# Kernel tuning notes

Hardware: AMD Instinct MI355X
Metric: run time of the kernel (lower is better)

The kernel has to match this reference:

```python
import jax, jax.numpy as jnp
import numpy as np

B, T, N, F_IN = 4, 16, 1000, 8
E = 8000
HID = 64
HEADS = 4
L = 5


def setup_inputs() -> dict:
    key = jax.random.key(0)
    ks = jax.random.split(key, 16)
    s = 0.1
    return {
        "x_seq": jax.random.normal(ks[0], (B, T, N, F_IN), dtype=jnp.float32),
        "edge_index": jax.random.randint(ks[1], (2, E), 0, N, dtype=jnp.int32),
        "edge_weight": jax.random.uniform(ks[2], (E,), dtype=jnp.float32),
        # input projection
        "W_in": jax.random.normal(ks[3], (F_IN, HID)) * s,
        "b_in": jnp.zeros((HID,), jnp.float32),
        # 5 stacked GATConv layers (heads=4, concat=False -> per-head dim = HID, mean over heads)
        "Wg": jax.random.normal(ks[4], (L, HID, HEADS * HID)) * s,
        "a_src": jax.random.normal(ks[5], (L, HEADS, HID)) * s,
        "a_dst": jax.random.normal(ks[6], (L, HEADS, HID)) * s,
        "bg": jnp.zeros((L, HID), jnp.float32),
        # GRU (input = N*HID flattened node features, torch gate order r,z,n)
        "W_ih": jax.random.normal(ks[7], (3 * HID, N * HID)) * 0.02,
        "W_hh": jax.random.normal(ks[8], (3 * HID, HID)) * s,
        "b_ih": jnp.zeros((3 * HID,), jnp.float32),
        "b_hh": jnp.zeros((3 * HID,), jnp.float32),
        # head: Linear(hidden_dim, num_nodes*pred_window) so out.view(B, N) works
        "W_fc": jax.random.normal(ks[9], (HID, N)) * s,
        "b_fc": jnp.zeros((N,), jnp.float32),
    }


def reference(x_seq, edge_index, edge_weight, W_in, b_in, Wg, a_src, a_dst, bg,
              W_ih, W_hh, b_ih, b_hh, W_fc, b_fc):
    Bb, Tt, Nn, Fin = x_seq.shape
    hid = W_in.shape[1]
    heads = a_src.shape[1]
    # PyG GATConv adds self-loops by default
    self_loops = jnp.arange(Nn, dtype=edge_index.dtype)
    src = jnp.concatenate([edge_index[0], self_loops])
    dst = jnp.concatenate([edge_index[1], self_loops])

    # input_fc over all (batch*seq*node) rows
    x = (x_seq.reshape(-1, Fin) @ W_in + b_in).reshape(Bb * Tt, Nn, hid)

    def gat_one(x_g, W, asrc, adst, b):
        h = (x_g @ W).reshape(Nn, heads, hid)            # [N,H,C]
        ls = (h * asrc).sum(-1)                          # [N,H] src attention terms
        ld = (h * adst).sum(-1)                          # [N,H] dst attention terms
        e = jax.nn.leaky_relu(ls[src] + ld[dst], 0.2)    # [E',H]
        m = jax.ops.segment_max(e, dst, num_segments=Nn)
        ex = jnp.exp(e - m[dst])
        den = jax.ops.segment_sum(ex, dst, num_segments=Nn)
        alpha = ex / (den[dst] + 1e-16)                  # softmax over incoming edges
        msg = alpha[:, :, None] * h[src]                 # [E',H,C]
        agg = jax.ops.segment_sum(msg, dst, num_segments=Nn)
        return agg.mean(axis=1) + b                      # concat=False -> mean heads

    for l in range(Wg.shape[0]):
        x = jax.nn.elu(jax.vmap(
            lambda xg, W=Wg[l], a1=a_src[l], a2=a_dst[l], b=bg[l]: gat_one(xg, W, a1, a2, b)
        )(x))

    # GRU over time, input = flattened node features per timestep
    seq = x.reshape(Bb, Tt, Nn * hid).transpose(1, 0, 2)  # [T,B,N*HID]

    def step(h, x_t):
        gi = x_t @ W_ih.T + b_ih
        gh = h @ W_hh.T + b_hh
        ir, iz, inn = jnp.split(gi, 3, axis=-1)
        hr, hz, hn = jnp.split(gh, 3, axis=-1)
        r = jax.nn.sigmoid(ir + hr)
        z = jax.nn.sigmoid(iz + hz)
        n = jnp.tanh(inn + r * hn)
        return (1.0 - z) * n + z * h, None

    h0 = jnp.zeros((Bb, hid), x_seq.dtype)
    hT, _ = jax.lax.scan(step, h0, seq)                  # last GRU output == final h
    return hT @ W_fc + b_fc                              # [B, N]
```

## Files before the change

### kernel.cpp

```cpp
#include <hip/hip_runtime.h>
#include <math.h>

#define NB 4
#define TT 16
#define NNODE 1000
#define FIN 8
#define EE 8000
#define EP 9000
#define EPAD 16384
#define HID 64
#define HEADS 4
#define NL 5
#define GG (NB*TT)
#define ROWS (GG*NNODE)
#define HCOL (HEADS*HID)
#define KGI (NNODE*HID)
#define GOUT 192
#define GIK 128
#define KSPLIT (KGI/GIK)
#define GOSZ (GG*GOUT)
#define WPSZ (8*4*64*8)

typedef unsigned short u16;
typedef __attribute__((ext_vector_type(8))) short short8;
typedef __attribute__((ext_vector_type(4))) float f32x4;

__device__ inline u16 f2bf(float f) {
    unsigned int u = __float_as_uint(f);
    unsigned int r = u + 0x7FFFu + ((u >> 16) & 1u);
    return (u16)(r >> 16);
}
__device__ inline float bf2f(u16 h) {
    return __uint_as_float(((unsigned int)h) << 16);
}
__device__ inline ushort4 bfhi4(float4 a) {
    ushort4 r; r.x = f2bf(a.x); r.y = f2bf(a.y); r.z = f2bf(a.z); r.w = f2bf(a.w); return r;
}
__device__ inline ushort4 bflo4(float4 a, ushort4 h) {
    ushort4 r;
    r.x = f2bf(a.x - bf2f(h.x)); r.y = f2bf(a.y - bf2f(h.y));
    r.z = f2bf(a.z - bf2f(h.z)); r.w = f2bf(a.w - bf2f(h.w));
    return r;
}

__global__ void k_build_edges(const int* __restrict__ eidx, int* __restrict__ src_e,
                              int* __restrict__ dst_e, int* __restrict__ deg, int* __restrict__ fill) {
    int i = blockIdx.x * blockDim.x + threadIdx.x;
    if (i < EP) {
        int s, d;
        if (i < EE) { s = eidx[i]; d = eidx[EE + i]; }
        else { s = i - EE; d = i - EE; }
        src_e[i] = s; dst_e[i] = d;
    }
    if (i < NNODE) { deg[i] = 0; fill[i] = 0; }
}

__global__ void k_csr_count(const int* __restrict__ dst_e, int* __restrict__ deg) {
    int i = blockIdx.x * blockDim.x + threadIdx.x;
    if (i < EP) atomicAdd(&deg[dst_e[i]], 1);
}

__global__ __launch_bounds__(256) void k_csr_scan(const int* __restrict__ deg, int* __restrict__ rowptr_p) {
    __shared__ int s[1024];
    int tid = threadIdx.x;
    for (int i = tid; i < 1024; i += 256) s[i] = (i < NNODE) ? ((deg[i] + 7) & ~7) : 0;
    __syncthreads();
    for (int off = 1; off < 1024; off <<= 1) {
        int t[4];
        #pragma unroll
        for (int q = 0; q < 4; q++) { int i = tid + 256 * q; t[q] = (i >= off) ? s[i - off] : 0; }
        __syncthreads();
        #pragma unroll
        for (int q = 0; q < 4; q++) { int i = tid + 256 * q; s[i] += t[q]; }
        __syncthreads();
    }
    for (int i = tid; i < NNODE; i += 256) rowptr_p[i + 1] = s[i];
    if (tid == 0) rowptr_p[0] = 0;
}

__global__ void k_csr_fill(const int* __restrict__ src_e, const int* __restrict__ dst_e,
                           const int* __restrict__ rowptr_p, const int* __restrict__ deg,
                           int* __restrict__ fill, int* __restrict__ csr_src) {
    int i = blockIdx.x * blockDim.x + threadIdx.x;
    if (i < EP) {
        int d = dst_e[i];
        int pos = atomicAdd(&fill[d], 1);
        csr_src[rowptr_p[d] + pos] = src_e[i];
    }
    if (i < NNODE) {
        int rs = rowptr_p[i], re = rowptr_p[i + 1];
        for (int j = rs + deg[i]; j < re; j++) csr_src[j] = i;
    }
}

__global__ void k_wa(const float* __restrict__ Wg, const float* __restrict__ a_src,
                     const float* __restrict__ a_dst, float* __restrict__ wa, float* __restrict__ wd) {
    int t = blockIdx.x * 256 + threadIdx.x;
    if (t >= 2 * NL * HID * HEADS) return;
    int kind = t >= NL * HID * HEADS;
    int u = t - kind * NL * HID * HEADS;
    int l = u >> 8;
    int rem = u & 255;
    int j = rem >> 2, hd = rem & 3;
    const float* a = (kind ? a_dst : a_src) + (size_t)l * HCOL + hd * HID;
    const float* Wl = Wg + (size_t)l * HID * HCOL + (size_t)j * HCOL + hd * HID;
    float acc = 0.f;
    #pragma unroll 8
    for (int c = 0; c < HID; c++) acc += Wl[c] * a[c];
    float* out = kind ? wd : wa;
    out[(size_t)l * HCOL + j * 4 + hd] = acc;
}

__global__ void k_wpack(const float* __restrict__ Wg, u16* __restrict__ wph, u16* __restrict__ wpl) {
    int t = blockIdx.x * 256 + threadIdx.x;
    if (t >= NL * WPSZ) return;
    int j    = t & 7;
    int lane = (t >> 3) & 63;
    int ct   = (t >> 9) & 3;
    int ks   = (t >> 11) & 7;
    int l    = t >> 14;
    int k = ks * 32 + (lane >> 4) * 8 + j;
    int c = ct * 16 + (lane & 15);
    float v = Wg[(size_t)l * HID * HCOL + (size_t)(k & 63) * HCOL + (k >> 6) * 64 + c];
    u16 h = f2bf(v);
    wph[t] = h;
    wpl[t] = f2bf(v - bf2f(h));
}

__global__ void k_input_fc(const float* __restrict__ xseq, const float4* __restrict__ Win4,
                           const float4* __restrict__ b_in4, const float4* __restrict__ wa04,
                           const float4* __restrict__ wd04, float4* __restrict__ x0,
                           float4* __restrict__ ls4, float4* __restrict__ ld4) {
    int idx = blockIdx.x * 256 + threadIdx.x;
    int r = idx >> 4, c4 = idx & 15;
    float4 acc = b_in4[c4];
    #pragma unroll
    for (int k = 0; k < FIN; k++) {
        float xv = xseq[r * FIN + k];
        float4 w = Win4[k * 16 + c4];
        acc.x += xv * w.x; acc.y += xv * w.y; acc.z += xv * w.z; acc.w += xv * w.w;
    }
    x0[idx] = acc;
    float xr[4] = {acc.x, acc.y, acc.z, acc.w};
    float4 pls = make_float4(0.f, 0.f, 0.f, 0.f);
    float4 pld = make_float4(0.f, 0.f, 0.f, 0.f);
    #pragma unroll
    for (int jj = 0; jj < 4; jj++) {
        float4 wa_j = wa04[c4 * 4 + jj];
        float4 wd_j = wd04[c4 * 4 + jj];
        pls.x += xr[jj] * wa_j.x; pls.y += xr[jj] * wa_j.y;
        pls.z += xr[jj] * wa_j.z; pls.w += xr[jj] * wa_j.w;
        pld.x += xr[jj] * wd_j.x; pld.y += xr[jj] * wd_j.y;
        pld.z += xr[jj] * wd_j.z; pld.w += xr[jj] * wd_j.w;
    }
    #pragma unroll
    for (int o = 1; o < 16; o <<= 1) {
        pls.x += __shfl_xor(pls.x, o, 64); pls.y += __shfl_xor(pls.y, o, 64);
        pls.z += __shfl_xor(pls.z, o, 64); pls.w += __shfl_xor(pls.w, o, 64);
        pld.x += __shfl_xor(pld.x, o, 64); pld.y += __shfl_xor(pld.y, o, 64);
        pld.z += __shfl_xor(pld.z, o, 64); pld.w += __shfl_xor(pld.w, o, 64);
    }
    if (c4 == 0) {
        ls4[r] = pls;
        ld4[r] = pld;
    }
}

__global__ __launch_bounds__(256) void k_aggx(const float4* __restrict__ x4, const float4* __restrict__ ls4,
                                              const float4* __restrict__ ld4, const int* __restrict__ rowptr_p,
                                              const int* __restrict__ csr_src, const int* __restrict__ deg,
                                              u16* __restrict__ yh, u16* __restrict__ yl) {
    __shared__ float s_e[4][4][264];
    __shared__ int   s_src[4][4][64];
    __shared__ float s_den[4][4][4];
    int b = blockIdx.x;
    int xcd = b & 7, s = b >> 3;
    int tid = threadIdx.x;
    int wid = tid >> 6, lane = tid & 63;
    int w = s * 4 + wid;
    int g = xcd + 8 * (w / 250);
    int n0 = (w % 250) * 4;
    int nsub = lane >> 4;
    int j0 = lane & 15;
    int n_s = n0 + nsub;
    int rs = rowptr_p[n_s];
    int dgp = rowptr_p[n_s + 1] - rs;
    int dg = deg[n_s];
    int dg16 = (dgp + 15) & ~15;
    if (dg16 > 64) dg16 = 64;
    if (dgp > 64) dgp = 64;
    if (dg > 64) dg = 64;
    float4 ldv = ld4[(size_t)g * NNODE + n_s];
    const float4* lsg = ls4 + (size_t)g * NNODE;

    float4 mx = make_float4(-1e30f, -1e30f, -1e30f, -1e30f);
    for (int base = 0; base < dg16; base += 16) {
        int j = base + j0;
        int sv = n_s;
        if (j < dgp) sv = csr_src[rs + j];
        s_src[wid][nsub][j] = sv;
        float4 lo = make_float4(-1e30f, -1e30f, -1e30f, -1e30f);
        if (j < dg) {
            float4 t = lsg[sv];
            t.x += ldv.x; t.y += ldv.y; t.z += ldv.z; t.w += ldv.w;
            t.x = fmaxf(t.x, 0.2f * t.x); t.y = fmaxf(t.y, 0.2f * t.y);
            t.z = fmaxf(t.z, 0.2f * t.z); t.w = fmaxf(t.w, 0.2f * t.w);
            lo = t;
            mx.x = fmaxf(mx.x, lo.x); mx.y = fmaxf(mx.y, lo.y);
            mx.z = fmaxf(mx.z, lo.z); mx.w = fmaxf(mx.w, lo.w);
        }
        *reinterpret_cast<float4*>(&s_e[wid][nsub][j * 4]) = lo;
    }
    #pragma unroll
    for (int o = 1; o < 16; o <<= 1) {
        mx.x = fmaxf(mx.x, __shfl_xor(mx.x, o, 64));
        mx.y = fmaxf(mx.y, __shfl_xor(mx.y, o, 64));
        mx.z = fmaxf(mx.z, __shfl_xor(mx.z, o, 64));
        mx.w = fmaxf(mx.w, __shfl_xor(mx.w, o, 64));
    }
    float4 den = make_float4(0.f, 0.f, 0.f, 0.f);
    for (int base = 0; base < dg16; base += 16) {
        int j = base + j0;
        float4 e = make_float4(0.f, 0.f, 0.f, 0.f);
        if (j < dg) {
            float4 lo = *reinterpret_cast<const float4*>(&s_e[wid][nsub][j * 4]);
            e.x = __expf(lo.x - mx.x);
            e.y = __expf(lo.y - mx.y);
            e.z = __expf(lo.z - mx.z);
            e.w = __expf(lo.w - mx.w);
        }
        den.x += e.x; den.y += e.y; den.z += e.z; den.w += e.w;
        *reinterpret_cast<float4*>(&s_e[wid][nsub][j * 4]) = e;
    }
    #pragma unroll
    for (int o = 1; o < 16; o <<= 1) {
        den.x += __shfl_xor(den.x, o, 64);
        den.y += __shfl_xor(den.y, o, 64);
        den.z += __shfl_xor(den.z, o, 64);
        den.w += __shfl_xor(den.w, o, 64);
    }
    if (j0 == 0) {
        *reinterpret_cast<float4*>(&s_den[wid][nsub][0]) = den;
    }

    int c4 = lane & 15;
    const float4* xg = x4 + (size_t)g * NNODE * 16 + c4;
    float4 a0 = make_float4(0.f, 0.f, 0.f, 0.f);
    float4 a1 = a0, a2 = a0, a3 = a0;
    const float* ep = &s_e[wid][nsub][0];
    const int* sp = &s_src[wid][nsub][0];
    int dg4 = (dg + 3) & ~3;
    int q = 0;
    for (; q + 8 <= dg4; q += 8) {
        int sj[8]; float4 ev[8], xv[8];
        #pragma unroll
        for (int u = 0; u < 8; u++) sj[u] = sp[q + u];
        #pragma unroll
        for (int u = 0; u < 8; u++) xv[u] = xg[(size_t)sj[u] * 16];
        #pragma unroll
        for (int u = 0; u < 8; u++) ev[u] = *reinterpret_cast<const float4*>(&ep[(q + u) * 4]);
        #pragma unroll
        for (int u = 0; u < 8; u++) {
            a0.x += ev[u].x * xv[u].x; a0.y += ev[u].x * xv[u].y;
            a0.z += ev[u].x * xv[u].z; a0.w += ev[u].x * xv[u].w;
            a1.x += ev[u].y * xv[u].x; a1.y += ev[u].y * xv[u].y;
            a1.z += ev[u].y * xv[u].z; a1.w += ev[u].y * xv[u].w;
            a2.x += ev[u].z * xv[u].x; a2.y += ev[u].z * xv[u].y;
            a2.z += ev[u].z * xv[u].z; a2.w += ev[u].z * xv[u].w;
            a3.x += ev[u].w * xv[u].x; a3.y += ev[u].w * xv[u].y;
            a3.z += ev[u].w * xv[u].z; a3.w += ev[u].w * xv[u].w;
        }
    }
    if (q < dg4) {
        int sj[4]; float4 ev[4], xv[4];
        #pragma unroll
        for (int u = 0; u < 4; u++) sj[u] = sp[q + u];
        #pragma unroll
        for (int u = 0; u < 4; u++) xv[u] = xg[(size_t)sj[u] * 16];
        #pragma unroll
        for (int u = 0; u < 4; u++) ev[u] = *reinterpret_cast<const float4*>(&ep[(q + u) * 4]);
        #pragma unroll
        for (int u = 0; u < 4; u++) {
            a0.x += ev[u].x * xv[u].x; a0.y += ev[u].x * xv[u].y;
            a0.z += ev[u].x * xv[u].z; a0.w += ev[u].x * xv[u].w;
            a1.x += ev[u].y * xv[u].x; a1.y += ev[u].y * xv[u].y;
            a1.z += ev[u].y * xv[u].z; a1.w += ev[u].y * xv[u].w;
            a2.x += ev[u].z * xv[u].x; a2.y += ev[u].z * xv[u].y;
            a2.z += ev[u].z * xv[u].z; a2.w += ev[u].z * xv[u].w;
            a3.x += ev[u].w * xv[u].x; a3.y += ev[u].w * xv[u].y;
            a3.z += ev[u].w * xv[u].z; a3.w += ev[u].w * xv[u].w;
        }
    }
    float4 dv = *reinterpret_cast<const float4*>(&s_den[wid][nsub][0]);
    float i0 = 1.f / (dv.x + 1e-16f), i1 = 1.f / (dv.y + 1e-16f);
    float i2 = 1.f / (dv.z + 1e-16f), i3 = 1.f / (dv.w + 1e-16f);
    a0.x *= i0; a0.y *= i0; a0.z *= i0; a0.w *= i0;
    a1.x *= i1; a1.y *= i1; a1.z *= i1; a1.w *= i1;
    a2.x *= i2; a2.y *= i2; a2.z *= i2; a2.w *= i2;
    a3.x *= i3; a3.y *= i3; a3.z *= i3; a3.w *= i3;
    size_t wb = ((size_t)g * NNODE + n_s) * 64 + c4;
    ushort4* YH = reinterpret_cast<ushort4*>(yh);
    ushort4* YL = reinterpret_cast<ushort4*>(yl);
    ushort4 h0 = bfhi4(a0), h1 = bfhi4(a1), h2 = bfhi4(a2), h3 = bfhi4(a3);
    YH[wb +  0] = h0; YL[wb +  0] = bflo4(a0, h0);
    YH[wb + 16] = h1; YL[wb + 16] = bflo4(a1, h1);
    YH[wb + 32] = h2; YL[wb + 32] = bflo4(a2, h2);
    YH[wb + 48] = h3; YL[wb + 48] = bflo4(a3, h3);
}

__global__ __launch_bounds__(256) void k_ygemm_mfma(const u16* __restrict__ yh, const u16* __restrict__ yl,
                                                    const u16* __restrict__ wph, const u16* __restrict__ wpl,
                                                    const float* __restrict__ bg, float* __restrict__ xout,
                                                    const float4* __restrict__ wa4, const float4* __restrict__ wd4,
                                                    float4* __restrict__ ls4, float4* __restrict__ ld4) {
    int tid = threadIdx.x;
    int wv = tid >> 6, lane = tid & 63;
    int r0w = blockIdx.x * 64 + wv * 16;
    int arow = lane & 15, kg = lane >> 4;

    f32x4 acc0 = {0.f, 0.f, 0.f, 0.f};
    f32x4 acc1 = {0.f, 0.f, 0.f, 0.f};
    f32x4 acc2 = {0.f, 0.f, 0.f, 0.f};
    f32x4 acc3 = {0.f, 0.f, 0.f, 0.f};

    const short8* ah8 = reinterpret_cast<const short8*>(yh + (size_t)(r0w + arow) * 256 + kg * 8);
    const short8* al8 = reinterpret_cast<const short8*>(yl + (size_t)(r0w + arow) * 256 + kg * 8);
    const short8* bh8 = reinterpret_cast<const short8*>(wph) + lane;
    const short8* bl8 = reinterpret_cast<const short8*>(wpl) + lane;

    #pragma unroll
    for (int ks = 0; ks < 8; ks++) {
        short8 ah = ah8[ks * 4];
        short8 al = al8[ks * 4];
        #pragma unroll
        for (int ct = 0; ct < 4; ct++) {
            short8 bh = bh8[(size_t)(ks * 4 + ct) * 64];
            short8 bl = bl8[(size_t)(ks * 4 + ct) * 64];
            f32x4* ac = (ct == 0) ? &acc0 : (ct == 1) ? &acc1 : (ct == 2) ? &acc2 : &acc3;
            *ac = __builtin_amdgcn_mfma_f32_16x16x32_bf16(ah, bh, *ac, 0, 0, 0);
            *ac = __builtin_amdgcn_mfma_f32_16x16x32_bf16(ah, bl, *ac, 0, 0, 0);
            *ac = __builtin_amdgcn_mfma_f32_16x16x32_bf16(al, bh, *ac, 0, 0, 0);
        }
    }

    float ev[4][4];
    #pragma unroll
    for (int ct = 0; ct < 4; ct++) {
        int c = ct * 16 + arow;
        float bc = bg[c];
        f32x4 a = (ct == 0) ? acc0 : (ct == 1) ? acc1 : (ct == 2) ? acc2 : acc3;
        #pragma unroll
        for (int r = 0; r < 4; r++) {
            float v = a[r] * 0.25f + bc;
            float e = v > 0.f ? v : expm1f(v);
            ev[ct][r] = e;
            xout[(size_t)(r0w + kg * 4 + r) * HID + c] = e;
        }
    }
    if (wa4) {
        #pragma unroll
        for (int r = 0; r < 4; r++) {
            float4 pls = make_float4(0.f, 0.f, 0.f, 0.f);
            float4 pld = make_float4(0.f, 0.f, 0.f, 0.f);
            #pragma unroll
            for (int ct = 0; ct < 4; ct++) {
                int c = ct * 16 + arow;
                float e = ev[ct][r];
                float4 wa_c = wa4[c];
                float4 wd_c = wd4[c];
                pls.x += e * wa_c.x; pls.y += e * wa_c.y;
                pls.z += e * wa_c.z; pls.w += e * wa_c.w;
                pld.x += e * wd_c.x; pld.y += e * wd_c.y;
                pld.z += e * wd_c.z; pld.w += e * wd_c.w;
            }
            #pragma unroll
            for (int o = 1; o < 16; o <<= 1) {
                pls.x += __shfl_xor(pls.x, o, 64); pls.y += __shfl_xor(pls.y, o, 64);
                pls.z += __shfl_xor(pls.z, o, 64); pls.w += __shfl_xor(pls.w, o, 64);
                pld.x += __shfl_xor(pld.x, o, 64); pld.y += __shfl_xor(pld.y, o, 64);
                pld.z += __shfl_xor(pld.z, o, 64); pld.w += __shfl_xor(pld.w, o, 64);
            }
            if (arow == 0) {
                int row = r0w + kg * 4 + r;
                ls4[row] = pls;
                ld4[row] = pld;
            }
        }
    }
}

__global__ __launch_bounds__(256) void k_gi_gemm(const float* __restrict__ x, const float* __restrict__ W_ih,
                                                 float* __restrict__ gip) {
    __shared__ float xs[32 * 68];
    __shared__ float ws[32 * 196];
    int k0 = blockIdx.x * GIK;
    int tid = threadIdx.x;
    int lane = tid & 63;
    int wv = tid >> 6;
    int tx = tid & 15, ty = tid >> 4;
    float4 accs[4][3];
    #pragma unroll
    for (int i = 0; i < 4; i++)
        #pragma unroll
        for (int j = 0; j < 3; j++) accs[i][j] = make_float4(0.f, 0.f, 0.f, 0.f);

    for (int kt = 0; kt < GIK / 32; kt++) {
        int kb = k0 + kt * 32;
        #pragma unroll
        for (int it = 0; it < 2; it++) {
            int kq = wv + 4 * it;
            float4 v = *reinterpret_cast<const float4*>(&x[(size_t)lane * KGI + kb + kq * 4]);
            int k = kq * 4;
            xs[(k + 0) * 68 + lane] = v.x;
            xs[(k + 1) * 68 + lane] = v.y;
            xs[(k + 2) * 68 + lane] = v.z;
            xs[(k + 3) * 68 + lane] = v.w;
        }
        #pragma unroll
        for (int cg = 0; cg < 3; cg++) {
            #pragma unroll
            for (int it = 0; it < 2; it++) {
                int kq = wv + 4 * it;
                int c = cg * 64 + lane;
                float4 v = *reinterpret_cast<const float4*>(&W_ih[(size_t)c * KGI + kb + kq * 4]);
                int k = kq * 4;
                ws[(k + 0) * 196 + c] = v.x;
                ws[(k + 1) * 196 + c] = v.y;
                ws[(k + 2) * 196 + c] = v.z;
                ws[(k + 3) * 196 + c] = v.w;
            }
        }
        __syncthreads();
        for (int kk = 0; kk < 32; kk++) {
            float4 xv = *reinterpret_cast<const float4*>(&xs[kk * 68 + ty * 4]);
            float4 w0 = *reinterpret_cast<const float4*>(&ws[kk * 196 + tx * 4]);
            float4 w1 = *reinterpret_cast<const float4*>(&ws[kk * 196 + 64 + tx * 4]);
            float4 w2 = *reinterpret_cast<const float4*>(&ws[kk * 196 + 128 + tx * 4]);
            #pragma unroll
            for (int i = 0; i < 4; i++) {
                float xi = (i == 0) ? xv.x : (i == 1) ? xv.y : (i == 2) ? xv.z : xv.w;
                accs[i][0].x += xi * w0.x; accs[i][0].y += xi * w0.y; accs[i][0].z += xi * w0.z; accs[i][0].w += xi * w0.w;
                accs[i][1].x += xi * w1.x; accs[i][1].y += xi * w1.y; accs[i][1].z += xi * w1.z; accs[i][1].w += xi * w1.w;
                accs[i][2].x += xi * w2.x; accs[i][2].y += xi * w2.y; accs[i][2].z += xi * w2.z; accs[i][2].w += xi * w2.w;
            }
        }
        __syncthreads();
    }
    float* out = gip + (size_t)blockIdx.x * GOSZ;
    #pragma unroll
    for (int i = 0; i < 4; i++)
        #pragma unroll
        for (int j = 0; j < 3; j++)
            *reinterpret_cast<float4*>(&out[(ty * 4 + i) * GOUT + j * 64 + tx * 4]) = accs[i][j];
}

__global__ void k_gi_reduce1(const float* __restrict__ gip, float* __restrict__ gip2) {
    int idx = blockIdx.x * 256 + threadIdx.x;
    const float* p = gip + (size_t)blockIdx.y * 50 * GOSZ + idx;
    float a = 0.f;
    #pragma unroll 5
    for (int s = 0; s < 50; s++) a += p[(size_t)s * GOSZ];
    gip2[blockIdx.y * GOSZ + idx] = a;
}

__global__ void k_gi_reduce2(const float* __restrict__ gip2, const float* __restrict__ b_ih,
                             float* __restrict__ gi) {
    int idx = blockIdx.x * 256 + threadIdx.x;
    float a = b_ih[idx % GOUT];
    #pragma unroll
    for (int y = 0; y < 10; y++) a += gip2[(size_t)y * GOSZ + idx];
    gi[idx] = a;
}

__global__ __launch_bounds__(192) void k_gru(const float* __restrict__ gi, const float* __restrict__ W_hh,
                                             const float* __restrict__ b_hh, float* __restrict__ hT) {
    __shared__ float hs[64];
    __shared__ float gh[192];
    int j = threadIdx.x;
    int b = blockIdx.x;
    float wrow[64];
    #pragma unroll
    for (int q = 0; q < 16; q++) {
        float4 v = *reinterpret_cast<const float4*>(&W_hh[(size_t)j * 64 + q * 4]);
        wrow[q * 4 + 0] = v.x; wrow[q * 4 + 1] = v.y;
        wrow[q * 4 + 2] = v.z; wrow[q * 4 + 3] = v.w;
    }
    float bj = b_hh[j];
    if (j < 64) hs[j] = 0.f;
    __syncthreads();
    for (int t = 0; t < TT; t++) {
        float a0 = 0.f, a1 = 0.f, a2 = 0.f, a3 = 0.f;
        #pragma unroll
        for (int q = 0; q < 16; q++) {
            float4 h4 = *reinterpret_cast<const float4*>(&hs[q * 4]);
            a0 += h4.x * wrow[q * 4 + 0];
            a1 += h4.y * wrow[q * 4 + 1];
            a2 += h4.z * wrow[q * 4 + 2];
            a3 += h4.w * wrow[q * 4 + 3];
        }
        gh[j] = bj + ((a0 + a1) + (a2 + a3));
        __syncthreads();
        if (j < 64) {
            int row = (b * TT + t) * GOUT;
            float ir = gi[row + j], iz = gi[row + 64 + j], in_ = gi[row + 128 + j];
            float r = 1.f / (1.f + expf(-(ir + gh[j])));
            float z = 1.f / (1.f + expf(-(iz + gh[64 + j])));
            float nv = tanhf(in_ + r * gh[128 + j]);
            hs[j] = (1.f - z) * nv + z * hs[j];
        }
        __syncthreads();
    }
    if (j < 64) hT[b * 64 + j] = hs[j];
}

__global__ void k_final(const float* __restrict__ hT, const float* __restrict__ W_fc,
                        const float* __restrict__ b_fc, float* __restrict__ out) {
    int idx = blockIdx.x * 256 + threadIdx.x;
    if (idx >= NB * NNODE) return;
    int b = idx / NNODE, n = idx % NNODE;
    float acc = b_fc[n];
    #pragma unroll
    for (int c = 0; c < HID; c++) acc += hT[b * HID + c] * W_fc[c * NNODE + n];
    out[idx] = acc;
}

extern "C" void kernel_launch(void* const* d_in, const int* in_sizes, int n_in,
                              void* d_out, int out_size, void* d_ws, size_t ws_size,
                              hipStream_t stream) {
    const float* x_seq  = (const float*)d_in[0];
    const int*   eidx   = (const int*)  d_in[1];
    const float* W_in   = (const float*)d_in[3];
    const float* b_in   = (const float*)d_in[4];
    const float* Wg     = (const float*)d_in[5];
    const float* a_src  = (const float*)d_in[6];
    const float* a_dst  = (const float*)d_in[7];
    const float* bg     = (const float*)d_in[8];
    const float* W_ih   = (const float*)d_in[9];
    const float* W_hh   = (const float*)d_in[10];
    const float* b_ih   = (const float*)d_in[11];
    const float* b_hh   = (const float*)d_in[12];
    const float* W_fc   = (const float*)d_in[13];
    const float* b_fc   = (const float*)d_in[14];
    float* out = (float*)d_out;

    float* wsf = (float*)d_ws;
    size_t off = 0;
    float* x0     = wsf + off; off += (size_t)ROWS * HID;
    float* ybuf   = wsf + off; off += (size_t)ROWS * HCOL;
    float* lsb    = wsf + off; off += (size_t)ROWS * HEADS;
    float* ldb    = wsf + off; off += (size_t)ROWS * HEADS;
    float* wab    = wsf + off; off += NL * HCOL;
    float* wdb    = wsf + off; off += NL * HCOL;
    float* gib    = wsf + off; off += GOSZ;
    float* hTb    = wsf + off; off += 256;
    u16* wphb     = (u16*)(wsf + off); off += NL * WPSZ / 2;
    u16* wplb     = (u16*)(wsf + off); off += NL * WPSZ / 2;
    int* ib = (int*)(wsf + off);
    int* src_e    = ib;          ib += EP;
    int* dst_e    = ib;          ib += EP;
    int* rowptr_p = ib;          ib += NNODE + 1;
    int* csr_src  = ib;          ib += EPAD;
    int* deg      = ib;          ib += NNODE;
    int* fill     = ib;          ib += NNODE;

    u16* yh = (u16*)ybuf;
    u16* yl = yh + (size_t)ROWS * HCOL;

    float* gip  = ybuf;
    float* gip2 = ybuf + (size_t)KSPLIT * GOSZ;

    k_build_edges<<<(EP + 255) / 256, 256, 0, stream>>>(eidx, src_e, dst_e, deg, fill);
    k_csr_count<<<(EP + 255) / 256, 256, 0, stream>>>(dst_e, deg);
    k_csr_scan<<<1, 256, 0, stream>>>(deg, rowptr_p);
    k_csr_fill<<<(EP + 255) / 256, 256, 0, stream>>>(src_e, dst_e, rowptr_p, deg, fill, csr_src);

    k_wa<<<10, 256, 0, stream>>>(Wg, a_src, a_dst, wab, wdb);
    k_wpack<<<(NL * WPSZ + 255) / 256, 256, 0, stream>>>(Wg, wphb, wplb);

    k_input_fc<<<ROWS * 16 / 256, 256, 0, stream>>>(
        x_seq, (const float4*)W_in, (const float4*)b_in,
        (const float4*)wab, (const float4*)wdb, (float4*)x0, (float4*)lsb, (float4*)ldb);

    for (int l = 0; l < NL; l++) {
        k_aggx<<<ROWS / 16, 256, 0, stream>>>(
            (const float4*)x0, (const float4*)lsb, (const float4*)ldb, rowptr_p, csr_src, deg,
            yh, yl);
        const float4* wa_next = (l + 1 < NL) ? (const float4*)(wab + (size_t)(l + 1) * HCOL) : nullptr;
        const float4* wd_next = (l + 1 < NL) ? (const float4*)(wdb + (size_t)(l + 1) * HCOL) : nullptr;
        k_ygemm_mfma<<<ROWS / 64, 256, 0, stream>>>(
            yh, yl, wphb + (size_t)l * WPSZ, wplb + (size_t)l * WPSZ,
            bg + (size_t)l * HID, x0,
            wa_next, wd_next, (float4*)lsb, (float4*)ldb);
    }

    k_gi_gemm<<<KSPLIT, 256, 0, stream>>>(x0, W_ih, gip);
    k_gi_reduce1<<<dim3(GOSZ / 256, 10), 256, 0, stream>>>(gip, gip2);
    k_gi_reduce2<<<GOSZ / 256, 256, 0, stream>>>(gip2, b_ih, gib);
    k_gru<<<4, 192, 0, stream>>>(gib, W_hh, b_hh, hTb);
    k_final<<<(NB * NNODE + 255) / 256, 256, 0, stream>>>(hTb, W_fc, b_fc, out);
}
```

Measured before the change: 432.4 us.

## Fuse GAT aggregation and MFMA projection into one kernel per layer

```diff
diff --git a/kernel.cpp b/kernel.cpp
--- a/kernel.cpp
+++ b/kernel.cpp
@@ -166,206 +166,208 @@
     }
 }
 
-__global__ __launch_bounds__(256) void k_aggx(const float4* __restrict__ x4, const float4* __restrict__ ls4,
-                                              const float4* __restrict__ ld4, const int* __restrict__ rowptr_p,
-                                              const int* __restrict__ csr_src, const int* __restrict__ deg,
-                                              u16* __restrict__ yh, u16* __restrict__ yl) {
+__global__ __launch_bounds__(256) void k_gat_fused(
+        const float4* __restrict__ x4, const float4* __restrict__ ls4, const float4* __restrict__ ld4,
+        const int* __restrict__ rowptr_p, const int* __restrict__ csr_src, const int* __restrict__ deg,
+        const u16* __restrict__ wph, const u16* __restrict__ wpl, const float* __restrict__ bg,
+        float* __restrict__ xout, const float4* __restrict__ wa4, const float4* __restrict__ wd4,
+        float4* __restrict__ lso4, float4* __restrict__ ldo4) {
+    __shared__ u16 yhs[32][264];
+    __shared__ u16 yls[32][264];
     __shared__ float s_e[4][4][264];
-    __shared__ int   s_src[4][4][64];
+    __shared__ unsigned short s_src[4][4][64];
     __shared__ float s_den[4][4][4];
     int b = blockIdx.x;
-    int xcd = b & 7, s = b >> 3;
+    int xcd = b & 7, sb = b >> 3;
+    int g = xcd + 8 * (sb >> 5);
+    int nb = (sb & 31) * 32;
     int tid = threadIdx.x;
     int wid = tid >> 6, lane = tid & 63;
-    int w = s * 4 + wid;
-    int g = xcd + 8 * (w / 250);
-    int n0 = (w % 250) * 4;
     int nsub = lane >> 4;
     int j0 = lane & 15;
-    int n_s = n0 + nsub;
-    int rs = rowptr_p[n_s];
-    int dgp = rowptr_p[n_s + 1] - rs;
-    int dg = deg[n_s];
-    int dg16 = (dgp + 15) & ~15;
-    if (dg16 > 64) dg16 = 64;
-    if (dgp > 64) dgp = 64;
-    if (dg > 64) dg = 64;
-    float4 ldv = ld4[(size_t)g * NNODE + n_s];
+    int c4 = lane & 15;
     const float4* lsg = ls4 + (size_t)g * NNODE;
-
-    float4 mx = make_float4(-1e30f, -1e30f, -1e30f, -1e30f);
-    for (int base = 0; base < dg16; base += 16) {
-        int j = base + j0;
-        int sv = n_s;
-        if (j < dgp) sv = csr_src[rs + j];
-        s_src[wid][nsub][j] = sv;
-        float4 lo = make_float4(-1e30f, -1e30f, -1e30f, -1e30f);
-        if (j < dg) {
-            float4 t = lsg[sv];
-            t.x += ldv.x; t.y += ldv.y; t.z += ldv.z; t.w += ldv.w;
-            t.x = fmaxf(t.x, 0.2f * t.x); t.y = fmaxf(t.y, 0.2f * t.y);
-            t.z = fmaxf(t.z, 0.2f * t.z); t.w = fmaxf(t.w, 0.2f * t.w);
-            lo = t;
-            mx.x = fmaxf(mx.x, lo.x); mx.y = fmaxf(mx.y, lo.y);
-            mx.z = fmaxf(mx.z, lo.z); mx.w = fmaxf(mx.w, lo.w);
-        }
-        *reinterpret_cast<float4*>(&s_e[wid][nsub][j * 4]) = lo;
-    }
-    #pragma unroll
-    for (int o = 1; o < 16; o <<= 1) {
-        mx.x = fmaxf(mx.x, __shfl_xor(mx.x, o, 64));
-        mx.y = fmaxf(mx.y, __shfl_xor(mx.y, o, 64));
-        mx.z = fmaxf(mx.z, __shfl_xor(mx.z, o, 64));
-        mx.w = fmaxf(mx.w, __shfl_xor(mx.w, o, 64));
-    }
-    float4 den = make_float4(0.f, 0.f, 0.f, 0.f);
-    for (int base = 0; base < dg16; base += 16) {
-        int j = base + j0;
-        float4 e = make_float4(0.f, 0.f, 0.f, 0.f);
-        if (j < dg) {
-            float4 lo = *reinterpret_cast<const float4*>(&s_e[wid][nsub][j * 4]);
-            e.x = __expf(lo.x - mx.x);
-            e.y = __expf(lo.y - mx.y);
-            e.z = __expf(lo.z - mx.z);
-            e.w = __expf(lo.w - mx.w);
-        }
-        den.x += e.x; den.y += e.y; den.z += e.z; den.w += e.w;
-        *reinterpret_cast<float4*>(&s_e[wid][nsub][j * 4]) = e;
-    }
-    #pragma unroll
-    for (int o = 1; o < 16; o <<= 1) {
-        den.x += __shfl_xor(den.x, o, 64);
-        den.y += __shfl_xor(den.y, o, 64);
-        den.z += __shfl_xor(den.z, o, 64);
-        den.w += __shfl_xor(den.w, o, 64);
-    }
-    if (j0 == 0) {
-        *reinterpret_cast<float4*>(&s_den[wid][nsub][0]) = den;
-    }
-
-    int c4 = lane & 15;
     const float4* xg = x4 + (size_t)g * NNODE * 16 + c4;
-    float4 a0 = make_float4(0.f, 0.f, 0.f, 0.f);
-    float4 a1 = a0, a2 = a0, a3 = a0;
-    const float* ep = &s_e[wid][nsub][0];
-    const int* sp = &s_src[wid][nsub][0];
-    int dg4 = (dg + 3) & ~3;
-    int q = 0;
-    for (; q + 8 <= dg4; q += 8) {
-        int sj[8]; float4 ev[8], xv[8];
-        #pragma unroll
-        for (int u = 0; u < 8; u++) sj[u] = sp[q + u];
-        #pragma unroll
-        for (int u = 0; u < 8; u++) xv[u] = xg[(size_t)sj[u] * 16];
-        #pragma unroll
-        for (int u = 0; u < 8; u++) ev[u] = *reinterpret_cast<const float4*>(&ep[(q + u) * 4]);
-        #pragma unroll
-        for (int u = 0; u < 8; u++) {
-            a0.x += ev[u].x * xv[u].x; a0.y += ev[u].x * xv[u].y;
-            a0.z += ev[u].x * xv[u].z; a0.w += ev[u].x * xv[u].w;
-            a1.x += ev[u].y * xv[u].x; a1.y += ev[u].y * xv[u].y;
-            a1.z += ev[u].y * xv[u].z; a1.w += ev[u].y * xv[u].w;
-            a2.x += ev[u].z * xv[u].x; a2.y += ev[u].z * xv[u].y;
-            a2.z += ev[u].z * xv[u].z; a2.w += ev[u].z * xv[u].w;
-            a3.x += ev[u].w * xv[u].x; a3.y += ev[u].w * xv[u].y;
-            a3.z += ev[u].w * xv[u].z; a3.w += ev[u].w * xv[u].w;
-        }
-    }
-    if (q < dg4) {
-        int sj[4]; float4 ev[4], xv[4];
-        #pragma unroll
-        for (int u = 0; u < 4; u++) sj[u] = sp[q + u];
-        #pragma unroll
-        for (int u = 0; u < 4; u++) xv[u] = xg[(size_t)sj[u] * 16];
-        #pragma unroll
-        for (int u = 0; u < 4; u++) ev[u] = *reinterpret_cast<const float4*>(&ep[(q + u) * 4]);
-        #pragma unroll
-        for (int u = 0; u < 4; u++) {
-            a0.x += ev[u].x * xv[u].x; a0.y += ev[u].x * xv[u].y;
-            a0.z += ev[u].x * xv[u].z; a0.w += ev[u].x * xv[u].w;
-            a1.x += ev[u].y * xv[u].x; a1.y += ev[u].y * xv[u].y;
-            a1.z += ev[u].y * xv[u].z; a1.w += ev[u].y * xv[u].w;
-            a2.x += ev[u].z * xv[u].x; a2.y += ev[u].z * xv[u].y;
-            a2.z += ev[u].z * xv[u].z; a2.w += ev[u].z * xv[u].w;
-            a3.x += ev[u].w * xv[u].x; a3.y += ev[u].w * xv[u].y;
-            a3.z += ev[u].w * xv[u].z; a3.w += ev[u].w * xv[u].w;
-        }
-    }
-    float4 dv = *reinterpret_cast<const float4*>(&s_den[wid][nsub][0]);
-    float i0 = 1.f / (dv.x + 1e-16f), i1 = 1.f / (dv.y + 1e-16f);
-    float i2 = 1.f / (dv.z + 1e-16f), i3 = 1.f / (dv.w + 1e-16f);
-    a0.x *= i0; a0.y *= i0; a0.z *= i0; a0.w *= i0;
-    a1.x *= i1; a1.y *= i1; a1.z *= i1; a1.w *= i1;
-    a2.x *= i2; a2.y *= i2; a2.z *= i2; a2.w *= i2;
-    a3.x *= i3; a3.y *= i3; a3.z *= i3; a3.w *= i3;
-    size_t wb = ((size_t)g * NNODE + n_s) * 64 + c4;
-    ushort4* YH = reinterpret_cast<ushort4*>(yh);
-    ushort4* YL = reinterpret_cast<ushort4*>(yl);
-    ushort4 h0 = bfhi4(a0), h1 = bfhi4(a1), h2 = bfhi4(a2), h3 = bfhi4(a3);
-    YH[wb +  0] = h0; YL[wb +  0] = bflo4(a0, h0);
-    YH[wb + 16] = h1; YL[wb + 16] = bflo4(a1, h1);
-    YH[wb + 32] = h2; YL[wb + 32] = bflo4(a2, h2);
-    YH[wb + 48] = h3; YL[wb + 48] = bflo4(a3, h3);
-}
-
-__global__ __launch_bounds__(256) void k_ygemm_mfma(const u16* __restrict__ yh, const u16* __restrict__ yl,
-                                                    const u16* __restrict__ wph, const u16* __restrict__ wpl,
-                                                    const float* __restrict__ bg, float* __restrict__ xout,
-                                                    const float4* __restrict__ wa4, const float4* __restrict__ wd4,
-                                                    float4* __restrict__ ls4, float4* __restrict__ ld4) {
-    int tid = threadIdx.x;
-    int wv = tid >> 6, lane = tid & 63;
-    int r0w = blockIdx.x * 64 + wv * 16;
+
+    for (int it2 = 0; it2 < 2; it2++) {
+        __syncthreads();
+        int n_l = wid * 8 + it2 * 4 + nsub;
+        int n_s = nb + n_l;
+        int valid = n_s < NNODE;
+        int n_c = valid ? n_s : (NNODE - 1);
+        int rs = rowptr_p[n_c];
+        int dgp = valid ? (rowptr_p[n_c + 1] - rs) : 0;
+        int dg = valid ? deg[n_c] : 0;
+        int dg16 = (dgp + 15) & ~15;
+        if (dg16 > 64) dg16 = 64;
+        if (dgp > 64) dgp = 64;
+        if (dg > 64) dg = 64;
+        float4 ldv = ld4[(size_t)g * NNODE + n_c];
+
+        float4 mx = make_float4(-1e30f, -1e30f, -1e30f, -1e30f);
+        for (int base = 0; base < dg16; base += 16) {
+            int j = base + j0;
+            int sv = n_c;
+            if (j < dgp) sv = csr_src[rs + j];
+            s_src[wid][nsub][j] = (unsigned short)sv;
+            float4 lo = make_float4(-1e30f, -1e30f, -1e30f, -1e30f);
+            if (j < dg) {
+                float4 t = lsg[sv];
+                t.x += ldv.x; t.y += ldv.y; t.z += ldv.z; t.w += ldv.w;
+                t.x = fmaxf(t.x, 0.2f * t.x); t.y = fmaxf(t.y, 0.2f * t.y);
+                t.z = fmaxf(t.z, 0.2f * t.z); t.w = fmaxf(t.w, 0.2f * t.w);
+                lo = t;
+                mx.x = fmaxf(mx.x, lo.x); mx.y = fmaxf(mx.y, lo.y);
+                mx.z = fmaxf(mx.z, lo.z); mx.w = fmaxf(mx.w, lo.w);
+            }
+            *reinterpret_cast<float4*>(&s_e[wid][nsub][j * 4]) = lo;
+        }
+        #pragma unroll
+        for (int o = 1; o < 16; o <<= 1) {
+            mx.x = fmaxf(mx.x, __shfl_xor(mx.x, o, 64));
+            mx.y = fmaxf(mx.y, __shfl_xor(mx.y, o, 64));
+            mx.z = fmaxf(mx.z, __shfl_xor(mx.z, o, 64));
+            mx.w = fmaxf(mx.w, __shfl_xor(mx.w, o, 64));
+        }
+        float4 den = make_float4(0.f, 0.f, 0.f, 0.f);
+        for (int base = 0; base < dg16; base += 16) {
+            int j = base + j0;
+            float4 e = make_float4(0.f, 0.f, 0.f, 0.f);
+            if (j < dg) {
+                float4 lo = *reinterpret_cast<const float4*>(&s_e[wid][nsub][j * 4]);
+                e.x = __expf(lo.x - mx.x);
+                e.y = __expf(lo.y - mx.y);
+                e.z = __expf(lo.z - mx.z);
+                e.w = __expf(lo.w - mx.w);
+            }
+            den.x += e.x; den.y += e.y; den.z += e.z; den.w += e.w;
+            *reinterpret_cast<float4*>(&s_e[wid][nsub][j * 4]) = e;
+        }
+        #pragma unroll
+        for (int o = 1; o < 16; o <<= 1) {
+            den.x += __shfl_xor(den.x, o, 64);
+            den.y += __shfl_xor(den.y, o, 64);
+            den.z += __shfl_xor(den.z, o, 64);
+            den.w += __shfl_xor(den.w, o, 64);
+        }
+        if (j0 == 0) *reinterpret_cast<float4*>(&s_den[wid][nsub][0]) = den;
+        __syncthreads();
+
+        float4 a0 = make_float4(0.f, 0.f, 0.f, 0.f);
+        float4 a1 = a0, a2 = a0, a3 = a0;
+        const float* ep = &s_e[wid][nsub][0];
+        const unsigned short* sp = &s_src[wid][nsub][0];
+        int dg4 = (dg + 3) & ~3;
+        int q = 0;
+        for (; q + 8 <= dg4; q += 8) {
+            int sj[8]; float4 ev[8], xv[8];
+            #pragma unroll
+            for (int u = 0; u < 8; u++) sj[u] = sp[q + u];
+            #pragma unroll
+            for (int u = 0; u < 8; u++) xv[u] = xg[(size_t)sj[u] * 16];
+            #pragma unroll
+            for (int u = 0; u < 8; u++) ev[u] = *reinterpret_cast<const float4*>(&ep[(q + u) * 4]);
+            #pragma unroll
+            for (int u = 0; u < 8; u++) {
+                a0.x += ev[u].x * xv[u].x; a0.y += ev[u].x * xv[u].y;
+                a0.z += ev[u].x * xv[u].z; a0.w += ev[u].x * xv[u].w;
+                a1.x += ev[u].y * xv[u].x; a1.y += ev[u].y * xv[u].y;
+                a1.z += ev[u].y * xv[u].z; a1.w += ev[u].y * xv[u].w;
+                a2.x += ev[u].z * xv[u].x; a2.y += ev[u].z * xv[u].y;
+                a2.z += ev[u].z * xv[u].z; a2.w += ev[u].z * xv[u].w;
+                a3.x += ev[u].w * xv[u].x; a3.y += ev[u].w * xv[u].y;
+                a3.z += ev[u].w * xv[u].z; a3.w += ev[u].w * xv[u].w;
+            }
+        }
+        if (q < dg4) {
+            int sj[4]; float4 ev[4], xv[4];
+            #pragma unroll
+            for (int u = 0; u < 4; u++) sj[u] = sp[q + u];
+            #pragma unroll
+            for (int u = 0; u < 4; u++) xv[u] = xg[(size_t)sj[u] * 16];
+            #pragma unroll
+            for (int u = 0; u < 4; u++) ev[u] = *reinterpret_cast<const float4*>(&ep[(q + u) * 4]);
+            #pragma unroll
+            for (int u = 0; u < 4; u++) {
+                a0.x += ev[u].x * xv[u].x; a0.y += ev[u].x * xv[u].y;
+                a0.z += ev[u].x * xv[u].z; a0.w += ev[u].x * xv[u].w;
+                a1.x += ev[u].y * xv[u].x; a1.y += ev[u].y * xv[u].y;
+                a1.z += ev[u].y * xv[u].z; a1.w += ev[u].y * xv[u].w;
+                a2.x += ev[u].z * xv[u].x; a2.y += ev[u].z * xv[u].y;
+                a2.z += ev[u].z * xv[u].z; a2.w += ev[u].z * xv[u].w;
+                a3.x += ev[u].w * xv[u].x; a3.y += ev[u].w * xv[u].y;
+                a3.z += ev[u].w * xv[u].z; a3.w += ev[u].w * xv[u].w;
+            }
+        }
+        float4 dv = *reinterpret_cast<const float4*>(&s_den[wid][nsub][0]);
+        float i0 = 1.f / (dv.x + 1e-16f), i1 = 1.f / (dv.y + 1e-16f);
+        float i2 = 1.f / (dv.z + 1e-16f), i3 = 1.f / (dv.w + 1e-16f);
+        a0.x *= i0; a0.y *= i0; a0.z *= i0; a0.w *= i0;
+        a1.x *= i1; a1.y *= i1; a1.z *= i1; a1.w *= i1;
+        a2.x *= i2; a2.y *= i2; a2.z *= i2; a2.w *= i2;
+        a3.x *= i3; a3.y *= i3; a3.z *= i3; a3.w *= i3;
+        ushort4 h0 = bfhi4(a0), h1 = bfhi4(a1), h2 = bfhi4(a2), h3 = bfhi4(a3);
+        *reinterpret_cast<ushort4*>(&yhs[n_l][0 * 64 + c4 * 4]) = h0;
+        *reinterpret_cast<ushort4*>(&yhs[n_l][1 * 64 + c4 * 4]) = h1;
+        *reinterpret_cast<ushort4*>(&yhs[n_l][2 * 64 + c4 * 4]) = h2;
+        *reinterpret_cast<ushort4*>(&yhs[n_l][3 * 64 + c4 * 4]) = h3;
+        *reinterpret_cast<ushort4*>(&yls[n_l][0 * 64 + c4 * 4]) = bflo4(a0, h0);
+        *reinterpret_cast<ushort4*>(&yls[n_l][1 * 64 + c4 * 4]) = bflo4(a1, h1);
+        *reinterpret_cast<ushort4*>(&yls[n_l][2 * 64 + c4 * 4]) = bflo4(a2, h2);
+        *reinterpret_cast<ushort4*>(&yls[n_l][3 * 64 + c4 * 4]) = bflo4(a3, h3);
+    }
+    __syncthreads();
+
+    int r0l = (wid & 1) * 16;
+    int ch = wid >> 1;
     int arow = lane & 15, kg = lane >> 4;
-
     f32x4 acc0 = {0.f, 0.f, 0.f, 0.f};
     f32x4 acc1 = {0.f, 0.f, 0.f, 0.f};
-    f32x4 acc2 = {0.f, 0.f, 0.f, 0.f};
-    f32x4 acc3 = {0.f, 0.f, 0.f, 0.f};
-
-    const short8* ah8 = reinterpret_cast<const short8*>(yh + (size_t)(r0w + arow) * 256 + kg * 8);
-    const short8* al8 = reinterpret_cast<const short8*>(yl + (size_t)(r0w + arow) * 256 + kg * 8);
     const short8* bh8 = reinterpret_cast<const short8*>(wph) + lane;
     const short8* bl8 = reinterpret_cast<const short8*>(wpl) + lane;
-
     #pragma unroll
     for (int ks = 0; ks < 8; ks++) {
-        short8 ah = ah8[ks * 4];
-        short8 al = al8[ks * 4];
-        #pragma unroll
-        for (int ct = 0; ct < 4; ct++) {
-            short8 bh = bh8[(size_t)(ks * 4 + ct) * 64];
-            short8 bl = bl8[(size_t)(ks * 4 + ct) * 64];
-            f32x4* ac = (ct == 0) ? &acc0 : (ct == 1) ? &acc1 : (ct == 2) ? &acc2 : &acc3;
+        short8 ah = *reinterpret_cast<const short8*>(&yhs[r0l + arow][ks * 32 + kg * 8]);
+        short8 al = *reinterpret_cast<const short8*>(&yls[r0l + arow][ks * 32 + kg * 8]);
+        #pragma unroll
+        for (int ctl = 0; ctl < 2; ctl++) {
+            int ctg = ch * 2 + ctl;
+            short8 bh = bh8[(size_t)(ks * 4 + ctg) * 64];
+            short8 bl = bl8[(size_t)(ks * 4 + ctg) * 64];
+            f32x4* ac = ctl ? &acc1 : &acc0;
             *ac = __builtin_amdgcn_mfma_f32_16x16x32_bf16(ah, bh, *ac, 0, 0, 0);
             *ac = __builtin_amdgcn_mfma_f32_16x16x32_bf16(ah, bl, *ac, 0, 0, 0);
             *ac = __builtin_amdgcn_mfma_f32_16x16x32_bf16(al, bh, *ac, 0, 0, 0);
         }
     }
 
-    float ev[4][4];
-    #pragma unroll
-    for (int ct = 0; ct < 4; ct++) {
-        int c = ct * 16 + arow;
+    float ev2[2][4];
+    #pragma unroll
+    for (int ctl = 0; ctl < 2; ctl++) {
+        int c = (ch * 2 + ctl) * 16 + arow;
         float bc = bg[c];
-        f32x4 a = (ct == 0) ? acc0 : (ct == 1) ? acc1 : (ct == 2) ? acc2 : acc3;
+        f32x4 a = ctl ? acc1 : acc0;
         #pragma unroll
         for (int r = 0; r < 4; r++) {
+            int node = nb + r0l + kg * 4 + r;
             float v = a[r] * 0.25f + bc;
             float e = v > 0.f ? v : expm1f(v);
-            ev[ct][r] = e;
-            xout[(size_t)(r0w + kg * 4 + r) * HID + c] = e;
+            ev2[ctl][r] = e;
+            if (node < NNODE)
+                xout[((size_t)g * NNODE + node) * HID + c] = e;
         }
     }
     if (wa4) {
+        float* s_part = &s_e[0][0][0];
+        __syncthreads();
         #pragma unroll
         for (int r = 0; r < 4; r++) {
             float4 pls = make_float4(0.f, 0.f, 0.f, 0.f);
             float4 pld = make_float4(0.f, 0.f, 0.f, 0.f);
             #pragma unroll
-            for (int ct = 0; ct < 4; ct++) {
-                int c = ct * 16 + arow;
-                float e = ev[ct][r];
+            for (int ctl = 0; ctl < 2; ctl++) {
+                int c = (ch * 2 + ctl) * 16 + arow;
+                float e = ev2[ctl][r];
                 float4 wa_c = wa4[c];
                 float4 wd_c = wd4[c];
                 pls.x += e * wa_c.x; pls.y += e * wa_c.y;
@@ -381,10 +383,18 @@
                 pld.z += __shfl_xor(pld.z, o, 64); pld.w += __shfl_xor(pld.w, o, 64);
             }
             if (arow == 0) {
-                int row = r0w + kg * 4 + r;
-                ls4[row] = pls;
-                ld4[row] = pld;
-            }
+                int rl = r0l + kg * 4 + r;
+                float4* p = reinterpret_cast<float4*>(&s_part[(ch * 32 + rl) * 8]);
+                p[0] = pls; p[1] = pld;
+            }
+        }
+        __syncthreads();
+        int rl = tid >> 3, cc = tid & 7;
+        int node = nb + rl;
+        if (node < NNODE) {
+            float v = s_part[rl * 8 + cc] + s_part[(32 + rl) * 8 + cc];
+            float* dst = (cc < 4) ? reinterpret_cast<float*>(lso4) : reinterpret_cast<float*>(ldo4);
+            dst[((size_t)g * NNODE + node) * 4 + (cc & 3)] = v;
         }
     }
 }
@@ -545,16 +555,20 @@
 
     float* wsf = (float*)d_ws;
     size_t off = 0;
-    float* x0     = wsf + off; off += (size_t)ROWS * HID;
-    float* ybuf   = wsf + off; off += (size_t)ROWS * HCOL;
-    float* lsb    = wsf + off; off += (size_t)ROWS * HEADS;
-    float* ldb    = wsf + off; off += (size_t)ROWS * HEADS;
+    float* x0a    = wsf + off; off += (size_t)ROWS * HID;
+    float* x0b    = wsf + off; off += (size_t)ROWS * HID;
+    float* lsa    = wsf + off; off += (size_t)ROWS * HEADS;
+    float* ldaf   = wsf + off; off += (size_t)ROWS * HEADS;
+    float* lsbf   = wsf + off; off += (size_t)ROWS * HEADS;
+    float* ldbf   = wsf + off; off += (size_t)ROWS * HEADS;
     float* wab    = wsf + off; off += NL * HCOL;
     float* wdb    = wsf + off; off += NL * HCOL;
     float* gib    = wsf + off; off += GOSZ;
     float* hTb    = wsf + off; off += 256;
     u16* wphb     = (u16*)(wsf + off); off += NL * WPSZ / 2;
     u16* wplb     = (u16*)(wsf + off); off += NL * WPSZ / 2;
+    float* gip    = wsf + off; off += (size_t)KSPLIT * GOSZ;
+    float* gip2   = wsf + off; off += 10 * GOSZ;
     int* ib = (int*)(wsf + off);
     int* src_e    = ib;          ib += EP;
     int* dst_e    = ib;          ib += EP;
@@ -563,12 +577,6 @@
     int* deg      = ib;          ib += NNODE;
     int* fill     = ib;          ib += NNODE;
 
-    u16* yh = (u16*)ybuf;
-    u16* yl = yh + (size_t)ROWS * HCOL;
-
-    float* gip  = ybuf;
-    float* gip2 = ybuf + (size_t)KSPLIT * GOSZ;
-
     k_build_edges<<<(EP + 255) / 256, 256, 0, stream>>>(eidx, src_e, dst_e, deg, fill);
     k_csr_count<<<(EP + 255) / 256, 256, 0, stream>>>(dst_e, deg);
     k_csr_scan<<<1, 256, 0, stream>>>(deg, rowptr_p);
@@ -579,21 +587,26 @@
 
     k_input_fc<<<ROWS * 16 / 256, 256, 0, stream>>>(
         x_seq, (const float4*)W_in, (const float4*)b_in,
-        (const float4*)wab, (const float4*)wdb, (float4*)x0, (float4*)lsb, (float4*)ldb);
-
+        (const float4*)wab, (const float4*)wdb, (float4*)x0a, (float4*)lsa, (float4*)ldaf);
+
+    float* xc = x0a;  float* xn = x0b;
+    float* lsc = lsa; float* ldc = ldaf;
+    float* lsn = lsbf; float* ldn = ldbf;
     for (int l = 0; l < NL; l++) {
-        k_aggx<<<ROWS / 16, 256, 0, stream>>>(
-            (const float4*)x0, (const float4*)lsb, (const float4*)ldb, rowptr_p, csr_src, deg,
-            yh, yl);
         const float4* wa_next = (l + 1 < NL) ? (const float4*)(wab + (size_t)(l + 1) * HCOL) : nullptr;
         const float4* wd_next = (l + 1 < NL) ? (const float4*)(wdb + (size_t)(l + 1) * HCOL) : nullptr;
-        k_ygemm_mfma<<<ROWS / 64, 256, 0, stream>>>(
-            yh, yl, wphb + (size_t)l * WPSZ, wplb + (size_t)l * WPSZ,
-            bg + (size_t)l * HID, x0,
-            wa_next, wd_next, (float4*)lsb, (float4*)ldb);
-    }
-
-    k_gi_gemm<<<KSPLIT, 256, 0, stream>>>(x0, W_ih, gip);
+        k_gat_fused<<<2048, 256, 0, stream>>>(
+            (const float4*)xc, (const float4*)lsc, (const float4*)ldc,
+            rowptr_p, csr_src, deg,
+            wphb + (size_t)l * WPSZ, wplb + (size_t)l * WPSZ, bg + (size_t)l * HID,
+            xn, wa_next, wd_next, (float4*)lsn, (float4*)ldn);
+        float* t;
+        t = xc; xc = xn; xn = t;
+        t = lsc; lsc = lsn; lsn = t;
+        t = ldc; ldc = ldn; ldn = t;
+    }
+
+    k_gi_gemm<<<KSPLIT, 256, 0, stream>>>(xc, W_ih, gip);
     k_gi_reduce1<<<dim3(GOSZ / 256, 10), 256, 0, stream>>>(gip, gip2);
     k_gi_reduce2<<<GOSZ / 256, 256, 0, stream>>>(gip2, b_ih, gib);
     k_gru<<<4, 192, 0, stream>>>(gib, W_hh, b_hh, hTb);
```

After: 414.4 us (median of 4 runs). 4.2% less time.
